# Kernel optimization log

Hardware: AMD Instinct MI355X
Metric: run time of the kernel (lower is better)

## Reference

```python
import jax, jax.numpy as jnp
import numpy as np

B, T, C, H = 4, 4096, 1024, 64

def setup_inputs() -> dict:
    key = jax.random.key(0)
    k1, k2, k3, k4 = jax.random.split(key, 4)
    x = jax.random.normal(k1, (B, T, C), dtype=jnp.float32)
    # Linear(n_embed, head_size, bias=False), stored as [in, out] for x @ W
    s = 1.0 / np.sqrt(C)
    Wq = jax.random.uniform(k2, (C, H), dtype=jnp.float32, minval=-s, maxval=s)
    Wk = jax.random.uniform(k3, (C, H), dtype=jnp.float32, minval=-s, maxval=s)
    Wv = jax.random.uniform(k4, (C, H), dtype=jnp.float32, minval=-s, maxval=s)
    return {"x": x, "Wq": Wq, "Wk": Wk, "Wv": Wv}

def reference(x, Wq, Wk, Wv):
    Bn, Tn, Cn = x.shape
    q = x @ Wq  # [B,T,H]
    k = x @ Wk  # [B,T,H]
    v = x @ Wv  # [B,T,H]
    # NOTE: original scales by C**-0.5 (embedding dim), not head_size**-0.5
    wei = jnp.einsum('bqh,bkh->bqk', q, k) * (Cn ** -0.5)  # [B,T,T]
    causal = jnp.tril(jnp.ones((Tn, Tn), dtype=bool))
    wei = jnp.where(causal, wei, -jnp.inf)
    wei = jax.nn.softmax(wei, axis=-1)
    out = jnp.einsum('bqk,bkh->bqh', wei, v)  # [B,T,H]
    return out
```

## Files before the change

kernel.cpp:

```cpp
#include <hip/hip_runtime.h>
#include <hip/hip_bf16.h>


#define B_DIM 4
#define T_DIM 4096
#define C_DIM 1024
#define H_DIM 64
#define SCALE2 0.0450842066f
#define KP 72

typedef __attribute__((ext_vector_type(8))) short bf8;
typedef __attribute__((ext_vector_type(4))) float f32x4;
typedef __attribute__((ext_vector_type(16))) float f32x16;

__device__ __forceinline__ float fast_exp2(float f) {
    return __builtin_amdgcn_exp2f(f);
}
__device__ __forceinline__ ushort f2bf(float f) {
    union { float f; uint u; } x; x.f = f;
    const uint u = x.u;
    return (ushort)((u + 0x7FFFu + ((u >> 16) & 1u)) >> 16);
}
__device__ __forceinline__ uint cvt_pk_bf16(float lo, float hi) {
    uint r;
    asm("v_cvt_pk_bf16_f32 %0, %1, %2" : "=v"(r) : "v"(lo), "v"(hi));
    return r;
}
__device__ __forceinline__ void permswapf(float& a, float& b) {
    asm volatile("v_permlane32_swap_b32 %0, %1" : "+v"(a), "+v"(b));
}
__device__ __forceinline__ void permswapu(uint& a, uint& b) {
    asm volatile("v_permlane32_swap_b32 %0, %1" : "+v"(a), "+v"(b));
}
__device__ __forceinline__ bf8 frag_from(uint w0, uint w1, uint w2, uint w3) {
    union { uint u[4]; bf8 f; } x;
    x.u[0] = w0; x.u[1] = w1; x.u[2] = w2; x.u[3] = w3;
    return x.f;
}

__global__ __launch_bounds__(256) void wt_kernel(
    const float* __restrict__ Wq, const float* __restrict__ Wk,
    const float* __restrict__ Wv, ushort* __restrict__ wtg)
{
    const int id  = blockIdx.x * 256 + threadIdx.x;
    const int col = id >> 7;
    const int k8  = (id & 127) * 8;
    const int m   = col >> 6, lc = col & 63;
    const float* W = (m == 0) ? Wq : (m == 1) ? Wk : Wv;
    ushort o[8];
    #pragma unroll
    for (int i = 0; i < 8; ++i)
        o[i] = f2bf(W[(size_t)(k8 + i) * H_DIM + lc]);
    *(bf8*)&wtg[(size_t)col * C_DIM + k8] = *(bf8*)o;
}

__global__ __launch_bounds__(256) void qkv_mfma_kernel(
    const float* __restrict__ x, const ushort* __restrict__ wtg,
    ushort* __restrict__ qo, ushort* __restrict__ ko, ushort* __restrict__ vo)
{
    __shared__ ushort xs[32][KP];
    __shared__ ushort wts[192][KP];
    const int t    = threadIdx.x;
    const int lane = t & 63, wave = t >> 6;
    const int g    = lane >> 4, lid = lane & 15;
    const size_t r0 = (size_t)blockIdx.x * 32;

    f32x4 acc[2][3] = {};

    const int xrow = t >> 3, xcol = (t & 7) * 8;
    float4 xr[2];
    bf8 wreg[6];

    xr[0] = *(const float4*)&x[(r0 + xrow) * C_DIM + xcol];
    xr[1] = *(const float4*)&x[(r0 + xrow) * C_DIM + xcol + 4];
    #pragma unroll
    for (int it = 0; it < 6; ++it) {
        const int n = t + it * 256;
        wreg[it] = *(const bf8*)&wtg[(size_t)(n >> 3) * C_DIM + (n & 7) * 8];
    }

    for (int kc = 0; kc < C_DIM / 64; ++kc) {
        __syncthreads();
        {
            uint p[4];
            p[0] = cvt_pk_bf16(xr[0].x, xr[0].y); p[1] = cvt_pk_bf16(xr[0].z, xr[0].w);
            p[2] = cvt_pk_bf16(xr[1].x, xr[1].y); p[3] = cvt_pk_bf16(xr[1].z, xr[1].w);
            *(bf8*)&xs[xrow][xcol] = *(bf8*)p;
            #pragma unroll
            for (int it = 0; it < 6; ++it) {
                const int n = t + it * 256;
                *(bf8*)&wts[n >> 3][(n & 7) * 8] = wreg[it];
            }
        }
        __syncthreads();
        if (kc + 1 < C_DIM / 64) {
            const int kb = (kc + 1) * 64;
            xr[0] = *(const float4*)&x[(r0 + xrow) * C_DIM + kb + xcol];
            xr[1] = *(const float4*)&x[(r0 + xrow) * C_DIM + kb + xcol + 4];
            #pragma unroll
            for (int it = 0; it < 6; ++it) {
                const int n = t + it * 256;
                wreg[it] = *(const bf8*)&wtg[(size_t)(n >> 3) * C_DIM + kb + (n & 7) * 8];
            }
        }
        #pragma unroll
        for (int ks = 0; ks < 2; ++ks) {
            const bf8 a0 = *(const bf8*)&xs[lid][ks * 32 + g * 8];
            const bf8 a1 = *(const bf8*)&xs[16 + lid][ks * 32 + g * 8];
            #pragma unroll
            for (int j = 0; j < 3; ++j) {
                const int ct = wave * 3 + j;
                const bf8 bb = *(const bf8*)&wts[ct * 16 + lid][ks * 32 + g * 8];
                acc[0][j] = __builtin_amdgcn_mfma_f32_16x16x32_bf16(a0, bb, acc[0][j], 0, 0, 0);
                acc[1][j] = __builtin_amdgcn_mfma_f32_16x16x32_bf16(a1, bb, acc[1][j], 0, 0, 0);
            }
        }
    }

    #pragma unroll
    for (int rt = 0; rt < 2; ++rt)
        #pragma unroll
        for (int j = 0; j < 3; ++j) {
            const int ct = wave * 3 + j;
            const int m  = ct >> 2, lc = (ct & 3) * 16 + lid;
            ushort* dst = (m == 0) ? qo : (m == 1) ? ko : vo;
            const float sc = (m == 0) ? SCALE2 : 1.f;
            #pragma unroll
            for (int r = 0; r < 4; ++r) {
                const size_t row = r0 + rt * 16 + 4 * g + r;
                dst[row * H_DIM + lc] = f2bf(acc[rt][j][r] * sc);
            }
        }
}

__global__ __launch_bounds__(256) void flash_mfma_kernel(
    const ushort* __restrict__ q, const ushort* __restrict__ k,
    const ushort* __restrict__ v, float* __restrict__ pO,
    float* __restrict__ pm, float* __restrict__ pl,
    float* __restrict__ out, int S, int nslots, int direct)
{
    const int qt  = 31 - blockIdx.y;
    const int c   = blockIdx.x;
    const int ntk = 2 * qt + 2;
    const int kt_begin = c * S;
    const int kt_end   = min((c + 1) * S, ntk);
    if (kt_begin >= kt_end) return;

    __shared__ ushort ks[64][KP];
    __shared__ ushort vt[64][KP];
    __shared__ float  fsh[4][32];
    __shared__ float  lsh[4][32];

    const int t    = threadIdx.x;
    const int lane = t & 63, wave = t >> 6;
    const int l31  = lane & 31, hi = lane >> 5;
    const int b    = blockIdx.z;
    const int bq0  = qt * 128;
    const int qrow0 = bq0 + wave * 32;
    const int ktw_max = (qrow0 + 31) >> 6;
    const size_t base = (size_t)b * T_DIM * H_DIM;

    bf8 qf[4];
    {
        const size_t qoff = base + (size_t)(qrow0 + l31) * H_DIM + hi * 8;
        #pragma unroll
        for (int kk = 0; kk < 4; ++kk)
            qf[kk] = *(const bf8*)&q[qoff + kk * 16];
    }

    f32x16 oa0 = {}, oa1 = {};
    float m_run = -1e29f, l_run = 0.f;

    const int krow = t >> 2, kc16 = (t & 3) * 16;
    const int vj = (t & 31) * 2, vc = (t >> 5) * 8;
    bf8 kr0, kr1, vr0, vr1;
    {
        const int kg = kt_begin * 64;
        kr0 = *(const bf8*)&k[base + (size_t)(kg + krow) * H_DIM + kc16];
        kr1 = *(const bf8*)&k[base + (size_t)(kg + krow) * H_DIM + kc16 + 8];
        vr0 = *(const bf8*)&v[base + (size_t)(kg + vj) * H_DIM + vc];
        vr1 = *(const bf8*)&v[base + (size_t)(kg + vj + 1) * H_DIM + vc];
    }

    #define BUILD_PA(dst, sv, bofs) do {                                   \
        uint a0_ = cvt_pk_bf16(sv[(bofs)+0], sv[(bofs)+1]);                \
        uint b0_ = cvt_pk_bf16(sv[(bofs)+4], sv[(bofs)+5]);                \
        uint a1_ = cvt_pk_bf16(sv[(bofs)+2], sv[(bofs)+3]);                \
        uint b1_ = cvt_pk_bf16(sv[(bofs)+6], sv[(bofs)+7]);                \
        permswapu(a0_, b0_); permswapu(a1_, b1_);                          \
        dst = frag_from(a0_, a1_, b0_, b1_);                               \
    } while (0)

    for (int kt64 = kt_begin; kt64 < kt_end; ++kt64) {
        __syncthreads();
        *(bf8*)&ks[krow][kc16]     = kr0;
        *(bf8*)&ks[krow][kc16 + 8] = kr1;
        #pragma unroll
        for (int i = 0; i < 8; ++i) {
            const uint pk = (uint)(ushort)vr0[i] | ((uint)(ushort)vr1[i] << 16);
            *(uint*)&vt[vc + i][vj] = pk;
        }
        __syncthreads();
        if (kt64 + 1 < kt_end) {
            const int kg = (kt64 + 1) * 64;
            kr0 = *(const bf8*)&k[base + (size_t)(kg + krow) * H_DIM + kc16];
            kr1 = *(const bf8*)&k[base + (size_t)(kg + krow) * H_DIM + kc16 + 8];
            vr0 = *(const bf8*)&v[base + (size_t)(kg + vj) * H_DIM + vc];
            vr1 = *(const bf8*)&v[base + (size_t)(kg + vj + 1) * H_DIM + vc];
        }
        if (kt64 > ktw_max) continue;

        f32x16 st0 = {}, st1 = {};
        #pragma unroll
        for (int kk = 0; kk < 4; ++kk) {
            const bf8 kfa = *(const bf8*)&ks[l31][kk * 16 + hi * 8];
            st0 = __builtin_amdgcn_mfma_f32_32x32x16_bf16(kfa, qf[kk], st0, 0, 0, 0);
        }
        #pragma unroll
        for (int kk = 0; kk < 4; ++kk) {
            const bf8 kfb = *(const bf8*)&ks[32 + l31][kk * 16 + hi * 8];
            st1 = __builtin_amdgcn_mfma_f32_32x32x16_bf16(kfb, qf[kk], st1, 0, 0, 0);
        }

        if (kt64 * 64 + 63 > qrow0) {
            const int qg  = qrow0 + l31;
            const int kb0 = kt64 * 64 + 4 * hi;
            #pragma unroll
            for (int r = 0; r < 16; ++r) {
                const int key0 = kb0 + (r & 3) + 8 * (r >> 2);
                if (key0 > qg)      st0[r] = -1e30f;
                if (key0 + 32 > qg) st1[r] = -1e30f;
            }
        }

        float mx = st0[0];
        #pragma unroll
        for (int r = 1; r < 16; ++r) mx = fmaxf(mx, st0[r]);
        #pragma unroll
        for (int r = 0; r < 16; ++r) mx = fmaxf(mx, st1[r]);
        { float ma = mx, mb = mx; permswapf(ma, mb); mx = fmaxf(ma, mb); }
        const bool nof = (mx <= m_run + 8.0f);
        const float mnew = nof ? m_run : mx;
        const float fsc  = nof ? 1.0f : fast_exp2(m_run - mnew);
        m_run = mnew;
        float ls = 0.f;
        #pragma unroll
        for (int r = 0; r < 16; ++r) { st0[r] = fast_exp2(st0[r] - mnew); ls += st0[r]; }
        #pragma unroll
        for (int r = 0; r < 16; ++r) { st1[r] = fast_exp2(st1[r] - mnew); ls += st1[r]; }
        { float la = ls, lb = ls; permswapf(la, lb); ls = la + lb; }
        l_run = l_run * fsc + ls;

        bf8 pa[4];
        BUILD_PA(pa[0], st0, 0);
        BUILD_PA(pa[1], st0, 8);
        BUILD_PA(pa[2], st1, 0);
        BUILD_PA(pa[3], st1, 8);

        if (!__all(nof)) {
            if (lane < 32) fsh[wave][l31] = fsc;
            #pragma unroll
            for (int j = 0; j < 4; ++j) {
                const float4 fb = *(const float4*)&fsh[wave][8 * j + 4 * hi];
                oa0[4*j+0] *= fb.x; oa0[4*j+1] *= fb.y; oa0[4*j+2] *= fb.z; oa0[4*j+3] *= fb.w;
                oa1[4*j+0] *= fb.x; oa1[4*j+1] *= fb.y; oa1[4*j+2] *= fb.z; oa1[4*j+3] *= fb.w;
            }
        }

        #pragma unroll
        for (int kk = 0; kk < 4; ++kk) {
            const bf8 vb0 = *(const bf8*)&vt[l31][kk * 16 + hi * 8];
            const bf8 vb1 = *(const bf8*)&vt[32 + l31][kk * 16 + hi * 8];
            oa0 = __builtin_amdgcn_mfma_f32_32x32x16_bf16(pa[kk], vb0, oa0, 0, 0, 0);
            oa1 = __builtin_amdgcn_mfma_f32_32x32x16_bf16(pa[kk], vb1, oa1, 0, 0, 0);
        }
    }
    #undef BUILD_PA

    if (direct) {
        if (lane < 32) lsh[wave][l31] = l_run;
        #pragma unroll
        for (int j = 0; j < 4; ++j) {
            const float4 lv = *(const float4*)&lsh[wave][8 * j + 4 * hi];
            const float iv[4] = {1.f / lv.x, 1.f / lv.y, 1.f / lv.z, 1.f / lv.w};
            #pragma unroll
            for (int rr = 0; rr < 4; ++rr) {
                const size_t rowoff = base + (size_t)(qrow0 + 8 * j + 4 * hi + rr) * H_DIM;
                out[rowoff + l31]      = oa0[4 * j + rr] * iv[rr];
                out[rowoff + 32 + l31] = oa1[4 * j + rr] * iv[rr];
            }
        }
    } else {
        const size_t u = ((size_t)b * 32 + qt) * nslots + c;
        float* po = pO + u * 8192;
        #pragma unroll
        for (int j = 0; j < 4; ++j)
            #pragma unroll
            for (int rr = 0; rr < 4; ++rr) {
                const int row = wave * 32 + 8 * j + 4 * hi + rr;
                po[(size_t)row * 64 + l31]      = oa0[4 * j + rr];
                po[(size_t)row * 64 + 32 + l31] = oa1[4 * j + rr];
            }
        if (lane < 32) {
            pm[u * 128 + wave * 32 + l31] = m_run;
            pl[u * 128 + wave * 32 + l31] = l_run;
        }
    }
}

__global__ __launch_bounds__(256) void combine_kernel(
    const float* __restrict__ pO, const float* __restrict__ pm,
    const float* __restrict__ pl, float* __restrict__ out,
    int S, int nslots)
{
    const int qt = blockIdx.x, b = blockIdx.y;
    const int ntk = 2 * qt + 2;
    const int nch = min(nslots, (ntk + S - 1) / S);
    const int t = threadIdx.x;
    const int row = t >> 1, seg = (t & 1) * 32;
    const size_t u0 = ((size_t)b * 32 + qt) * nslots;

    float M = -1e30f;
    for (int cc = 0; cc < nch; ++cc)
        M = fmaxf(M, pm[(u0 + cc) * 128 + row]);
    float L = 0.f, alpha[8];
    for (int cc = 0; cc < nch; ++cc) {
        alpha[cc] = fast_exp2(pm[(u0 + cc) * 128 + row] - M);
        L += pl[(u0 + cc) * 128 + row] * alpha[cc];
    }
    const float inv = 1.f / L;

    float4 o[8] = {};
    for (int cc = 0; cc < nch; ++cc) {
        const float a = alpha[cc];
        #pragma unroll
        for (int j = 0; j < 8; ++j) {
            const float4 p = *(const float4*)&pO[(u0 + cc) * 8192 +
                                                 (size_t)row * 64 + seg + j * 4];
            o[j].x += p.x * a; o[j].y += p.y * a;
            o[j].z += p.z * a; o[j].w += p.w * a;
        }
    }
    const size_t ob = (size_t)b * T_DIM * H_DIM + (size_t)(qt * 128 + row) * H_DIM + seg;
    #pragma unroll
    for (int j = 0; j < 8; ++j) {
        float4 r;
        r.x = o[j].x * inv; r.y = o[j].y * inv;
        r.z = o[j].z * inv; r.w = o[j].w * inv;
        *(float4*)&out[ob + j * 4] = r;
    }
}

extern "C" void kernel_launch(void* const* d_in, const int* in_sizes, int n_in,
                              void* d_out, int out_size, void* d_ws, size_t ws_size,
                              hipStream_t stream)
{
    const float* x  = (const float*)d_in[0];
    const float* Wq = (const float*)d_in[1];
    const float* Wk = (const float*)d_in[2];
    const float* Wv = (const float*)d_in[3];
    float* out = (float*)d_out;

    const size_t MB = 1u << 20;
    char* ws = (char*)d_ws;
    ushort* qb  = (ushort*)(ws);
    ushort* kb  = (ushort*)(ws + 2 * MB);
    ushort* vb  = (ushort*)(ws + 4 * MB);
    ushort* wtg = (ushort*)(ws + 6 * MB);
    float*  pO  = (float*)(ws + 7 * MB);

    int nslots, S;
    if      (ws_size >= 41 * MB) { nslots = 8; S = 8;  }
    else if (ws_size >= 24 * MB) { nslots = 4; S = 16; }
    else if (ws_size >= 16 * MB) { nslots = 2; S = 32; }
    else                         { nslots = 1; S = 64; }
    const int direct = (nslots == 1);
    float* pm = pO + (size_t)nslots * 1048576;
    float* pl = pm + (size_t)nslots * 16384;

    hipLaunchKernelGGL(wt_kernel, dim3(96), dim3(256), 0, stream, Wq, Wk, Wv, wtg);
    hipLaunchKernelGGL(qkv_mfma_kernel, dim3((B_DIM * T_DIM) / 32), dim3(256),
                       0, stream, x, wtg, qb, kb, vb);
    hipLaunchKernelGGL(flash_mfma_kernel, dim3(nslots, T_DIM / 128, B_DIM), dim3(256),
                       0, stream, qb, kb, vb, pO, pm, pl, out, S, nslots, direct);
    if (!direct)
        hipLaunchKernelGGL(combine_kernel, dim3(T_DIM / 128, B_DIM), dim3(256),
                           0, stream, pO, pm, pl, out, S, nslots);
}
```

Baseline: 77.59 us.

## Double-buffer QKV projection, load weights to registers, add 16-slot split-K

The QKV projection kernel drops the shared-memory staging of the weight tiles. Each wave now loads its B fragments straight from global memory into registers, and the x tile is double-buffered in LDS so the next chunk loads while MFMAs run on the current one. Separately, the flash kernel's rescale threshold is tightened from 8 to 4. When the workspace is large enough, a 16-slot key-split configuration is added and the 2-slot tier is removed. This trades more partial-output traffic and combine work for more parallelism, and adds more synchronisation points per loop iteration.

After: 101.1 us. +30.3%, slower.

```diff
diff --git a/kernel.cpp b/kernel.cpp
--- a/kernel.cpp
+++ b/kernel.cpp
@@ -58,64 +58,75 @@
     const float* __restrict__ x, const ushort* __restrict__ wtg,
     ushort* __restrict__ qo, ushort* __restrict__ ko, ushort* __restrict__ vo)
 {
-    __shared__ ushort xs[32][KP];
-    __shared__ ushort wts[192][KP];
+    __shared__ ushort xs[2][32][KP];
     const int t    = threadIdx.x;
     const int lane = t & 63, wave = t >> 6;
     const int g    = lane >> 4, lid = lane & 15;
     const size_t r0 = (size_t)blockIdx.x * 32;
 
     f32x4 acc[2][3] = {};
-
     const int xrow = t >> 3, xcol = (t & 7) * 8;
-    float4 xr[2];
-    bf8 wreg[6];
-
-    xr[0] = *(const float4*)&x[(r0 + xrow) * C_DIM + xcol];
-    xr[1] = *(const float4*)&x[(r0 + xrow) * C_DIM + xcol + 4];
-    #pragma unroll
-    for (int it = 0; it < 6; ++it) {
-        const int n = t + it * 256;
-        wreg[it] = *(const bf8*)&wtg[(size_t)(n >> 3) * C_DIM + (n & 7) * 8];
-    }
-
-    for (int kc = 0; kc < C_DIM / 64; ++kc) {
-        __syncthreads();
-        {
-            uint p[4];
-            p[0] = cvt_pk_bf16(xr[0].x, xr[0].y); p[1] = cvt_pk_bf16(xr[0].z, xr[0].w);
-            p[2] = cvt_pk_bf16(xr[1].x, xr[1].y); p[3] = cvt_pk_bf16(xr[1].z, xr[1].w);
-            *(bf8*)&xs[xrow][xcol] = *(bf8*)p;
-            #pragma unroll
-            for (int it = 0; it < 6; ++it) {
-                const int n = t + it * 256;
-                *(bf8*)&wts[n >> 3][(n & 7) * 8] = wreg[it];
-            }
-        }
-        __syncthreads();
-        if (kc + 1 < C_DIM / 64) {
-            const int kb = (kc + 1) * 64;
-            xr[0] = *(const float4*)&x[(r0 + xrow) * C_DIM + kb + xcol];
-            xr[1] = *(const float4*)&x[(r0 + xrow) * C_DIM + kb + xcol + 4];
-            #pragma unroll
-            for (int it = 0; it < 6; ++it) {
-                const int n = t + it * 256;
-                wreg[it] = *(const bf8*)&wtg[(size_t)(n >> 3) * C_DIM + kb + (n & 7) * 8];
-            }
-        }
-        #pragma unroll
-        for (int ks = 0; ks < 2; ++ks) {
-            const bf8 a0 = *(const bf8*)&xs[lid][ks * 32 + g * 8];
-            const bf8 a1 = *(const bf8*)&xs[16 + lid][ks * 32 + g * 8];
-            #pragma unroll
-            for (int j = 0; j < 3; ++j) {
-                const int ct = wave * 3 + j;
-                const bf8 bb = *(const bf8*)&wts[ct * 16 + lid][ks * 32 + g * 8];
-                acc[0][j] = __builtin_amdgcn_mfma_f32_16x16x32_bf16(a0, bb, acc[0][j], 0, 0, 0);
-                acc[1][j] = __builtin_amdgcn_mfma_f32_16x16x32_bf16(a1, bb, acc[1][j], 0, 0, 0);
-            }
-        }
-    }
+    float4 xrA[2], xrB[2];
+    bf8 wfA[6], wfB[6];
+
+    #define LOAD_WF(buf, kc_) do {                                           \
+        _Pragma("unroll")                                                    \
+        for (int ks = 0; ks < 2; ++ks)                                       \
+            _Pragma("unroll")                                                \
+            for (int j = 0; j < 3; ++j)                                      \
+                buf[ks * 3 + j] = *(const bf8*)&wtg[                         \
+                    (size_t)((wave * 3 + j) * 16 + lid) * C_DIM +            \
+                    (kc_) * 64 + ks * 32 + g * 8];                           \
+    } while (0)
+    #define LOAD_XR(buf, kc_) do {                                           \
+        buf[0] = *(const float4*)&x[(r0 + xrow) * C_DIM + (kc_) * 64 + xcol];     \
+        buf[1] = *(const float4*)&x[(r0 + xrow) * C_DIM + (kc_) * 64 + xcol + 4]; \
+    } while (0)
+    #define WRITE_XS(sb, buf) do {                                           \
+        uint p_[4];                                                          \
+        p_[0] = cvt_pk_bf16(buf[0].x, buf[0].y);                             \
+        p_[1] = cvt_pk_bf16(buf[0].z, buf[0].w);                             \
+        p_[2] = cvt_pk_bf16(buf[1].x, buf[1].y);                             \
+        p_[3] = cvt_pk_bf16(buf[1].z, buf[1].w);                             \
+        *(bf8*)&xs[sb][xrow][xcol] = *(bf8*)p_;                              \
+    } while (0)
+    #define MFMA_STEP(sb, wf) do {                                           \
+        _Pragma("unroll")                                                    \
+        for (int ks = 0; ks < 2; ++ks) {                                     \
+            const bf8 a0 = *(const bf8*)&xs[sb][lid][ks * 32 + g * 8];       \
+            const bf8 a1 = *(const bf8*)&xs[sb][16 + lid][ks * 32 + g * 8];  \
+            _Pragma("unroll")                                                \
+            for (int j = 0; j < 3; ++j) {                                    \
+                acc[0][j] = __builtin_amdgcn_mfma_f32_16x16x32_bf16(a0, wf[ks * 3 + j], acc[0][j], 0, 0, 0); \
+                acc[1][j] = __builtin_amdgcn_mfma_f32_16x16x32_bf16(a1, wf[ks * 3 + j], acc[1][j], 0, 0, 0); \
+            }                                                                \
+        }                                                                    \
+    } while (0)
+
+    LOAD_XR(xrA, 0);
+    LOAD_WF(wfA, 0);
+    LOAD_XR(xrB, 1);
+    WRITE_XS(0, xrA);
+    __syncthreads();
+
+    for (int kc = 0; kc < C_DIM / 64; kc += 2) {
+        if (kc + 2 < C_DIM / 64) LOAD_XR(xrA, kc + 2);
+        LOAD_WF(wfB, kc + 1);
+        MFMA_STEP(0, wfA);
+        __syncthreads();
+        WRITE_XS(1, xrB);
+        __syncthreads();
+        if (kc + 3 < C_DIM / 64) LOAD_XR(xrB, kc + 3);
+        if (kc + 2 < C_DIM / 64) LOAD_WF(wfA, kc + 2);
+        MFMA_STEP(1, wfB);
+        __syncthreads();
+        if (kc + 2 < C_DIM / 64) WRITE_XS(0, xrA);
+        __syncthreads();
+    }
+    #undef MFMA_STEP
+    #undef WRITE_XS
+    #undef LOAD_XR
+    #undef LOAD_WF
 
     #pragma unroll
     for (int rt = 0; rt < 2; ++rt)
@@ -239,7 +250,7 @@
         #pragma unroll
         for (int r = 0; r < 16; ++r) mx = fmaxf(mx, st1[r]);
         { float ma = mx, mb = mx; permswapf(ma, mb); mx = fmaxf(ma, mb); }
-        const bool nof = (mx <= m_run + 8.0f);
+        const bool nof = (mx <= m_run + 4.0f);
         const float mnew = nof ? m_run : mx;
         const float fsc  = nof ? 1.0f : fast_exp2(m_run - mnew);
         m_run = mnew;
@@ -323,7 +334,7 @@
     float M = -1e30f;
     for (int cc = 0; cc < nch; ++cc)
         M = fmaxf(M, pm[(u0 + cc) * 128 + row]);
-    float L = 0.f, alpha[8];
+    float L = 0.f, alpha[16];
     for (int cc = 0; cc < nch; ++cc) {
         alpha[cc] = fast_exp2(pm[(u0 + cc) * 128 + row] - M);
         L += pl[(u0 + cc) * 128 + row] * alpha[cc];
@@ -370,10 +381,10 @@
     float*  pO  = (float*)(ws + 7 * MB);
 
     int nslots, S;
-    if      (ws_size >= 41 * MB) { nslots = 8; S = 8;  }
-    else if (ws_size >= 24 * MB) { nslots = 4; S = 16; }
-    else if (ws_size >= 16 * MB) { nslots = 2; S = 32; }
-    else                         { nslots = 1; S = 64; }
+    if      (ws_size >= 80 * MB) { nslots = 16; S = 4; }
+    else if (ws_size >= 41 * MB) { nslots = 8;  S = 8; }
+    else if (ws_size >= 24 * MB) { nslots = 4;  S = 16; }
+    else                         { nslots = 1;  S = 64; }
     const int direct = (nslots == 1);
     float* pm = pO + (size_t)nslots * 1048576;
     float* pl = pm + (size_t)nslots * 16384;
```
